# Kernel tuning notes

Measured on AMD Instinct MI355X. Metric: run time of the kernel, lower is better.

## Reference

```python
import jax, jax.numpy as jnp
import numpy as np

B, CIN, REL, OUT, SH, H, W = 8, 256, 16, 64, 8, 56, 56
HW = H * W
K = 7          # window size
DIL = 2        # dilation
EPS = 1e-5


def conv1x1(x, w, b=None):
    # x: [B,C,h,w], w: [O,C]
    y = jnp.einsum('oc,bchw->bohw', w, x)
    if b is not None:
        y = y + b[None, :, None, None]
    return y


def bn_eval(x, g, b, m, v):
    scale = g / jnp.sqrt(v + EPS)
    return x * scale[None, :, None, None] + (b - m * scale)[None, :, None, None]


def unfold49(x, pad_reflect, pad_zero):
    # x: [B,C,H,W] -> [B,C,49,H,W]; 7x7 window, dilation 2, stride 1.
    if pad_reflect:
        x = jnp.pad(x, ((0, 0), (0, 0), (pad_reflect, pad_reflect), (pad_reflect, pad_reflect)), mode='reflect')
    if pad_zero:
        x = jnp.pad(x, ((0, 0), (0, 0), (pad_zero, pad_zero), (pad_zero, pad_zero)))
    patches = [x[:, :, DIL * i:DIL * i + H, DIL * j:DIL * j + W]
               for i in range(K) for j in range(K)]
    return jnp.stack(patches, axis=2)


def setup_inputs() -> dict:
    key = jax.random.key(0)
    ks = jax.random.split(key, 12)
    s_in = 1.0 / np.sqrt(CIN)
    inp = {
        'x': jax.random.normal(ks[0], (B, CIN, H, W), jnp.float32),
        'w1': jax.random.normal(ks[1], (REL, CIN), jnp.float32) * s_in,
        'b1': jax.random.normal(ks[2], (REL,), jnp.float32) * 0.01,
        'w2': jax.random.normal(ks[3], (REL, CIN), jnp.float32) * s_in,
        'b2': jax.random.normal(ks[4], (REL,), jnp.float32) * 0.01,
        'w3': jax.random.normal(ks[5], (OUT, CIN), jnp.float32) * s_in,
        'b3': jax.random.normal(ks[6], (OUT,), jnp.float32) * 0.01,
        'bn1_g': jax.random.uniform(ks[7], (REL * (K * K + 1),), jnp.float32, 0.5, 1.5),
        'bn1_b': jax.random.normal(ks[8], (REL * (K * K + 1),), jnp.float32) * 0.01,
        'bn1_m': jnp.zeros((REL * (K * K + 1),), jnp.float32),
        'bn1_v': jnp.ones((REL * (K * K + 1),), jnp.float32),
        'wcw1': jax.random.normal(ks[9], (OUT // SH, REL * (K * K + 1)), jnp.float32) * (1.0 / np.sqrt(REL * 50)),
        'bn2_g': jax.random.uniform(ks[10], (OUT // SH,), jnp.float32, 0.5, 1.5),
        'bn2_b': jnp.zeros((OUT // SH,), jnp.float32),
        'bn2_m': jnp.zeros((OUT // SH,), jnp.float32),
        'bn2_v': jnp.ones((OUT // SH,), jnp.float32),
        'wcw2': jax.random.normal(ks[11], (K * K * OUT // SH, OUT // SH), jnp.float32) * (1.0 / np.sqrt(OUT // SH)),
        'bcw2': jnp.zeros((K * K * OUT // SH,), jnp.float32),
    }
    return inp


def reference(x, w1, b1, w2, b2, w3, b3, bn1_g, bn1_b, bn1_m, bn1_v,
              wcw1, bn2_g, bn2_b, bn2_m, bn2_v, wcw2, bcw2):
    x1 = conv1x1(x, w1, b1)                      # [B,REL,H,W]
    x2 = conv1x1(x, w2, b2)                      # [B,REL,H,W]
    x3 = conv1x1(x, w3, b3)                      # [B,OUT,H,W]

    # x1 -> [B,REL,1,HW]
    x1f = x1.reshape(B, REL, 1, HW)
    # x2: ReflectionPad2d(2) then Unfold(7, dilation=2, padding=4) -> [B,REL*49,1,HW]
    x2u = unfold49(x2, pad_reflect=2, pad_zero=4).reshape(B, REL * K * K, 1, HW)

    cat = jnp.concatenate([x1f, x2u], axis=1)    # [B, REL*50, 1, HW]
    t = jax.nn.relu(bn_eval(cat, bn1_g, bn1_b, bn1_m, bn1_v))
    t = conv1x1(t, wcw1)                         # [B, OUT/SH, 1, HW], no bias
    t = jax.nn.relu(bn_eval(t, bn2_g, bn2_b, bn2_m, bn2_v))
    wmap = conv1x1(t, wcw2, bcw2)                # [B, 49*OUT/SH, 1, HW]
    wmap = wmap.reshape(B, OUT // SH, K * K, HW)  # channel layout wc*49+k

    # Aggregation(7, 1, 6, 2, pad_mode=1): reflect-pad 6, 7x7 dilated unfold,
    # out[b,c,n] = sum_k unf[b,c,k,n] * w[b, c//SH, k, n]
    x3u = unfold49(x3, pad_reflect=6, pad_zero=0).reshape(B, OUT // SH, SH, K * K, HW)
    out = jnp.einsum('bgskn,bgkn->bgsn', x3u, wmap).reshape(B, OUT, H, W)
    return out
```

## Files before the change

kernel.cpp:

```cpp
#include <hip/hip_runtime.h>
#include <hip/hip_bf16.h>

#define HW    3136
#define HH    56
#define NCIN  256
#define KK    49
#define PH    68
#define PP    (PH*PH)

#define OFF_WT    0
#define OFF_BCAT  24576
#define OFF_SSH   24672
#define OFF_WC1T  26272
#define OFF_B2F   32672
#define OFF_X1    32768
#define OFF_X2P   434176
#define OFF_X3P   1026048
#define OFF_TB    3393536

__global__ __launch_bounds__(256) void kprep(
    const float* __restrict__ w1, const float* __restrict__ b1,
    const float* __restrict__ w2, const float* __restrict__ b2,
    const float* __restrict__ w3, const float* __restrict__ b3,
    const float* __restrict__ bn1g, const float* __restrict__ bn1b,
    const float* __restrict__ bn1m, const float* __restrict__ bn1v,
    const float* __restrict__ wcw1,
    const float* __restrict__ bn2g, const float* __restrict__ bn2b,
    const float* __restrict__ bn2m, const float* __restrict__ bn2v,
    float* __restrict__ ws)
{
    int idx = blockIdx.x * 256 + threadIdx.x;
    if (idx < 24576) {
        int o = idx >> 8, c = idx & 255;
        float v = (o < 16) ? w1[o * 256 + c]
                : (o < 32) ? w2[(o - 16) * 256 + c]
                           : w3[(o - 32) * 256 + c];
        ws[OFF_WT + c * 96 + o] = v;
    }
    int i2 = idx - 24576;
    if (i2 >= 0 && i2 < 96) {
        float v = (i2 < 16) ? b1[i2] : (i2 < 32) ? b2[i2 - 16] : b3[i2 - 32];
        ws[OFF_BCAT + i2] = v;
    }
    int i3 = idx - 24672;
    if (i3 >= 0 && i3 < 800) {
        float s = bn1g[i3] / sqrtf(bn1v[i3] + 1e-5f);
        ws[OFF_SSH + 2 * i3]     = s;
        ws[OFF_SSH + 2 * i3 + 1] = bn1b[i3] - bn1m[i3] * s;
    }
    int i4 = idx - 25472;
    if (i4 >= 0 && i4 < 6400) {
        int j = i4 >> 3, g = i4 & 7;
        float s2 = bn2g[g] / sqrtf(bn2v[g] + 1e-5f);
        ws[OFF_WC1T + i4] = wcw1[g * 800 + j] * s2;
    }
    int i5 = idx - 31872;
    if (i5 >= 0 && i5 < 8) {
        float s2 = bn2g[i5] / sqrtf(bn2v[i5] + 1e-5f);
        ws[OFF_B2F + i5] = bn2b[i5] - bn2m[i5] * s2;
    }
    int i6 = idx - 31880;
    if (i6 >= 0 && i6 < 8 * 16 * PP) {
        ws[OFF_X2P + i6] = 0.f;
    }
}

__global__ __launch_bounds__(512) void kconv(
    const float* __restrict__ x, const float* __restrict__ wT,
    const float* __restrict__ bcat, float* __restrict__ x1out,
    float* __restrict__ x2pad, float* __restrict__ x3pad)
{
    __shared__ float xl[64][64];
    const int tid = threadIdx.x;
    const int l   = tid & 63;
    const int wv  = __builtin_amdgcn_readfirstlane(tid >> 6);
    const int b   = blockIdx.x / 49;
    const int hw0 = (blockIdx.x % 49) * 64;
    const int ob  = wv * 12;

    float acc[12];
    const float* bc = bcat + ob;
#pragma unroll
    for (int i = 0; i < 12; ++i) acc[i] = bc[i];

    const float* xb = x + (size_t)b * NCIN * HW + hw0;

    for (int cc = 0; cc < 4; ++cc) {
        __syncthreads();
#pragma unroll
        for (int i = 0; i < 8; ++i)
            xl[i * 8 + wv][l] = xb[(size_t)(cc * 64 + i * 8 + wv) * HW + l];
        __syncthreads();

        const float* wp = wT + (cc * 64) * 96 + ob;
#pragma unroll 4
        for (int k = 0; k < 64; ++k) {
            float xv = xl[k][l];
            const float4* wq = (const float4*)(wp + k * 96);
            float4 A = wq[0], B = wq[1], C = wq[2];
            acc[0]  = fmaf(xv, A.x, acc[0]);  acc[1]  = fmaf(xv, A.y, acc[1]);
            acc[2]  = fmaf(xv, A.z, acc[2]);  acc[3]  = fmaf(xv, A.w, acc[3]);
            acc[4]  = fmaf(xv, B.x, acc[4]);  acc[5]  = fmaf(xv, B.y, acc[5]);
            acc[6]  = fmaf(xv, B.z, acc[6]);  acc[7]  = fmaf(xv, B.w, acc[7]);
            acc[8]  = fmaf(xv, C.x, acc[8]);  acc[9]  = fmaf(xv, C.y, acc[9]);
            acc[10] = fmaf(xv, C.z, acc[10]); acc[11] = fmaf(xv, C.w, acc[11]);
        }
    }

    const int n  = hw0 + l;
    const int y  = n / HH;
    const int xx = n - y * HH;
    const int p0 = y + 6, q0 = xx + 6;
    const int yr3 = (y >= 1 && y <= 6) ? 6 - y : ((y >= 49 && y <= 54) ? 116 - y : -1);
    const int xr3 = (xx >= 1 && xx <= 6) ? 6 - xx : ((xx >= 49 && xx <= 54) ? 116 - xx : -1);
    const int yr2 = (y == 1 || y == 2) ? 6 - y : ((y == 53 || y == 54) ? 116 - y : -1);
    const int xr2 = (xx == 1 || xx == 2) ? 6 - xx : ((xx == 53 || xx == 54) ? 116 - xx : -1);

#pragma unroll
    for (int i = 0; i < 12; ++i) {
        const int ch = ob + i;
        const float v = acc[i];
        if (ch < 16) {
            x1out[((size_t)b * 16 + ch) * HW + n] = v;
        } else if (ch < 32) {
            float* pl = x2pad + ((size_t)b * 16 + (ch - 16)) * PP;
            pl[p0 * PH + q0] = v;
            if (yr2 >= 0)              pl[yr2 * PH + q0]  = v;
            if (xr2 >= 0)              pl[p0 * PH + xr2]  = v;
            if (yr2 >= 0 && xr2 >= 0)  pl[yr2 * PH + xr2] = v;
        } else {
            float* pl = x3pad + ((size_t)b * 64 + (ch - 32)) * PP;
            pl[p0 * PH + q0] = v;
            if (yr3 >= 0)              pl[yr3 * PH + q0]  = v;
            if (xr3 >= 0)              pl[p0 * PH + xr3]  = v;
            if (yr3 >= 0 && xr3 >= 0)  pl[yr3 * PH + xr3] = v;
        }
    }
}

__global__ __launch_bounds__(512) void kt(
    const float* __restrict__ x1, const float* __restrict__ x2pad,
    const float* __restrict__ ssh, const float* __restrict__ wc1t,
    const float* __restrict__ b2f, float* __restrict__ tbuf)
{
    __shared__ float red[8][8][64];
    const int tid = threadIdx.x;
    const int w   = __builtin_amdgcn_readfirstlane(tid >> 6);
    const int l   = tid & 63;
    const int b   = blockIdx.x / 49;
    const int nb  = (blockIdx.x % 49) * 64;
    const int n   = nb + l;
    const int y   = n / HH;
    const int xx  = n - y * HH;
    const int pbase = y * PH + xx;

    const float* x1b = x1 + (size_t)b * 16 * HW + n;
    const float* x2b = x2pad + (size_t)b * 16 * PP + pbase;

    float acc[8];
#pragma unroll
    for (int g = 0; g < 8; ++g) acc[g] = 0.f;

    const int u0 = (50 * w) >> 3;
    const int u1 = (50 * (w + 1)) >> 3;

#pragma unroll 2
    for (int u = u0; u < u1; ++u) {
        if (u == 0) {
#pragma unroll
            for (int r = 0; r < 16; ++r) {
                float v = x1b[(size_t)r * HW];
                float2 ss = *(const float2*)(ssh + 2 * r);
                v = fmaxf(fmaf(v, ss.x, ss.y), 0.f);
                const float4* wq = (const float4*)(wc1t + r * 8);
                float4 A = wq[0], Bv = wq[1];
                acc[0] = fmaf(v, A.x, acc[0]);  acc[1] = fmaf(v, A.y, acc[1]);
                acc[2] = fmaf(v, A.z, acc[2]);  acc[3] = fmaf(v, A.w, acc[3]);
                acc[4] = fmaf(v, Bv.x, acc[4]); acc[5] = fmaf(v, Bv.y, acc[5]);
                acc[6] = fmaf(v, Bv.z, acc[6]); acc[7] = fmaf(v, Bv.w, acc[7]);
            }
        } else {
            const int kk = __builtin_amdgcn_readfirstlane(u - 1);
            const int i  = kk / 7;
            const int jj = kk - i * 7;
            const float* xp = x2b + i * (2 * PH) + jj * 2;
#pragma unroll
            for (int r = 0; r < 16; ++r) {
                const int j = 16 + r * KK + kk;
                float v = xp[(size_t)r * PP];
                float2 ss = *(const float2*)(ssh + 2 * j);
                v = fmaxf(fmaf(v, ss.x, ss.y), 0.f);
                const float4* wq = (const float4*)(wc1t + j * 8);
                float4 A = wq[0], Bv = wq[1];
                acc[0] = fmaf(v, A.x, acc[0]);  acc[1] = fmaf(v, A.y, acc[1]);
                acc[2] = fmaf(v, A.z, acc[2]);  acc[3] = fmaf(v, A.w, acc[3]);
                acc[4] = fmaf(v, Bv.x, acc[4]); acc[5] = fmaf(v, Bv.y, acc[5]);
                acc[6] = fmaf(v, Bv.z, acc[6]); acc[7] = fmaf(v, Bv.w, acc[7]);
            }
        }
    }

#pragma unroll
    for (int g = 0; g < 8; ++g) red[w][g][l] = acc[g];
    __syncthreads();

    {
        const int g  = tid >> 6;
        const int px = tid & 63;
        float s = b2f[g];
#pragma unroll
        for (int ww = 0; ww < 8; ++ww) s += red[ww][g][px];
        tbuf[((size_t)b * 8 + g) * HW + nb + px] = fmaxf(s, 0.f);
    }
}

__global__ __launch_bounds__(512) void kagg(
    const float* __restrict__ x3pad, const float* __restrict__ tbuf,
    const float* __restrict__ wcw2, const float* __restrict__ bcw2,
    float* __restrict__ out)
{
    const int tid  = threadIdx.x;
    const int g    = __builtin_amdgcn_readfirstlane(tid >> 6);
    const int lane = tid & 63;
    const int sh   = lane >> 5;
    const int pp   = lane & 31;
    const int b    = blockIdx.x / 49;
    const int nb   = (blockIdx.x % 49) * 64;
    const int n0   = nb + pp * 2;
    const int y    = n0 / HH;
    const int xx   = n0 - y * HH;
    const int pbase = y * PH + xx;

    float t0[8], t1[8];
#pragma unroll
    for (int e = 0; e < 8; ++e) {
        float2 tv = *(const float2*)(tbuf + ((size_t)b * 8 + e) * HW + n0);
        t0[e] = tv.x; t1[e] = tv.y;
    }

    float2 acc[4];
#pragma unroll
    for (int s = 0; s < 4; ++s) acc[s] = make_float2(0.f, 0.f);

    const float* x3b = x3pad + ((size_t)b * 64 + g * 8 + sh * 4) * PP + pbase;
    const float* wr  = wcw2 + (size_t)g * KK * 8;
    const float* br  = bcw2 + (size_t)g * KK;

#pragma unroll 1
    for (int i = 0; i < 7; ++i) {
        const float* xrow = x3b + i * (2 * PH);
#pragma unroll
        for (int jj = 0; jj < 7; ++jj) {
            const int k = i * 7 + jj;
            float w0 = br[k], w1 = w0;
            const float* wk = wr + k * 8;
#pragma unroll
            for (int e = 0; e < 8; ++e) {
                float we = wk[e];
                w0 = fmaf(t0[e], we, w0);
                w1 = fmaf(t1[e], we, w1);
            }
#pragma unroll
            for (int s = 0; s < 4; ++s) {
                float2 xv = *(const float2*)(xrow + (size_t)s * PP + jj * 2);
                acc[s].x = fmaf(xv.x, w0, acc[s].x);
                acc[s].y = fmaf(xv.y, w1, acc[s].y);
            }
        }
    }

    float* op = out + ((size_t)b * 64 + g * 8 + sh * 4) * HW + n0;
#pragma unroll
    for (int s = 0; s < 4; ++s)
        *(float2*)(op + (size_t)s * HW) = acc[s];
}

extern "C" void kernel_launch(void* const* d_in, const int* in_sizes, int n_in,
                              void* d_out, int out_size, void* d_ws, size_t ws_size,
                              hipStream_t stream) {
    const float* x    = (const float*)d_in[0];
    const float* w1   = (const float*)d_in[1];
    const float* b1   = (const float*)d_in[2];
    const float* w2   = (const float*)d_in[3];
    const float* b2   = (const float*)d_in[4];
    const float* w3   = (const float*)d_in[5];
    const float* b3   = (const float*)d_in[6];
    const float* bn1g = (const float*)d_in[7];
    const float* bn1b = (const float*)d_in[8];
    const float* bn1m = (const float*)d_in[9];
    const float* bn1v = (const float*)d_in[10];
    const float* wcw1 = (const float*)d_in[11];
    const float* bn2g = (const float*)d_in[12];
    const float* bn2b = (const float*)d_in[13];
    const float* bn2m = (const float*)d_in[14];
    const float* bn2v = (const float*)d_in[15];
    const float* wcw2 = (const float*)d_in[16];
    const float* bcw2 = (const float*)d_in[17];

    float* ws = (float*)d_ws;

    kprep<<<2437, 256, 0, stream>>>(w1, b1, w2, b2, w3, b3,
                                    bn1g, bn1b, bn1m, bn1v, wcw1,
                                    bn2g, bn2b, bn2m, bn2v, ws);
    kconv<<<392, 512, 0, stream>>>(x, ws + OFF_WT, ws + OFF_BCAT,
                                   ws + OFF_X1, ws + OFF_X2P, ws + OFF_X3P);
    kt<<<392, 512, 0, stream>>>(ws + OFF_X1, ws + OFF_X2P,
                                ws + OFF_SSH, ws + OFF_WC1T, ws + OFF_B2F,
                                ws + OFF_TB);
    kagg<<<392, 512, 0, stream>>>(ws + OFF_X3P, ws + OFF_TB, wcw2, bcw2,
                                  (float*)d_out);
}
```

Measured before the change: 77.78 us.

## Widen kt/kagg blocks to 1024 threads, pack weight tables, move pad zeroing into kconv

After: 81.42 us. 4.7% more time.

```diff
diff --git a/kernel.cpp b/kernel.cpp
--- a/kernel.cpp
+++ b/kernel.cpp
@@ -10,13 +10,13 @@
 
 #define OFF_WT    0
 #define OFF_BCAT  24576
-#define OFF_SSH   24672
-#define OFF_WC1T  26272
-#define OFF_B2F   32672
-#define OFF_X1    32768
-#define OFF_X2P   434176
-#define OFF_X3P   1026048
-#define OFF_TB    3393536
+#define OFF_TAB   24672
+#define OFF_WTAB  34272
+#define OFF_B2F   38976
+#define OFF_X1    39040
+#define OFF_X2P   440448
+#define OFF_X3P   1032320
+#define OFF_TB    3399808
 
 __global__ __launch_bounds__(256) void kprep(
     const float* __restrict__ w1, const float* __restrict__ b1,
@@ -27,6 +27,7 @@
     const float* __restrict__ wcw1,
     const float* __restrict__ bn2g, const float* __restrict__ bn2b,
     const float* __restrict__ bn2m, const float* __restrict__ bn2v,
+    const float* __restrict__ wcw2, const float* __restrict__ bcw2,
     float* __restrict__ ws)
 {
     int idx = blockIdx.x * 256 + threadIdx.x;
@@ -43,25 +44,35 @@
         ws[OFF_BCAT + i2] = v;
     }
     int i3 = idx - 24672;
-    if (i3 >= 0 && i3 < 800) {
-        float s = bn1g[i3] / sqrtf(bn1v[i3] + 1e-5f);
-        ws[OFF_SSH + 2 * i3]     = s;
-        ws[OFF_SSH + 2 * i3 + 1] = bn1b[i3] - bn1m[i3] * s;
-    }
-    int i4 = idx - 25472;
-    if (i4 >= 0 && i4 < 6400) {
-        int j = i4 >> 3, g = i4 & 7;
-        float s2 = bn2g[g] / sqrtf(bn2v[g] + 1e-5f);
-        ws[OFF_WC1T + i4] = wcw1[g * 800 + j] * s2;
-    }
-    int i5 = idx - 31872;
+    if (i3 >= 0 && i3 < 9600) {
+        int row = i3 / 12, c = i3 - row * 12;
+        int uu = row >> 4, r = row & 15;
+        int j = (uu < 49) ? (16 + r * KK + uu) : r;
+        float val = 0.f;
+        if (c == 0) {
+            val = bn1g[j] / sqrtf(bn1v[j] + 1e-5f);
+        } else if (c == 1) {
+            float s = bn1g[j] / sqrtf(bn1v[j] + 1e-5f);
+            val = bn1b[j] - bn1m[j] * s;
+        } else if (c < 10) {
+            int e = c - 2;
+            float s2 = bn2g[e] / sqrtf(bn2v[e] + 1e-5f);
+            val = wcw1[e * 800 + j] * s2;
+        }
+        ws[OFF_TAB + i3] = val;
+    }
+    int i4 = idx - 34272;
+    if (i4 >= 0 && i4 < 4704) {
+        int row = i4 / 12, c = i4 - row * 12;
+        float val = 0.f;
+        if (c == 0)      val = bcw2[row];
+        else if (c < 9)  val = wcw2[row * 8 + (c - 1)];
+        ws[OFF_WTAB + i4] = val;
+    }
+    int i5 = idx - 38976;
     if (i5 >= 0 && i5 < 8) {
         float s2 = bn2g[i5] / sqrtf(bn2v[i5] + 1e-5f);
         ws[OFF_B2F + i5] = bn2b[i5] - bn2m[i5] * s2;
-    }
-    int i6 = idx - 31880;
-    if (i6 >= 0 && i6 < 8 * 16 * PP) {
-        ws[OFF_X2P + i6] = 0.f;
     }
 }
 
@@ -77,6 +88,18 @@
     const int b   = blockIdx.x / 49;
     const int hw0 = (blockIdx.x % 49) * 64;
     const int ob  = wv * 12;
+
+    {
+        int z = (blockIdx.x % 49) * 336 + tid;
+        if (tid < 336 && z < 16384) {
+            int ch = z >> 10, cell = z & 1023;
+            int p, q;
+            if (cell < 272)      { p = cell / 68;          q = cell - p * 68; }
+            else if (cell < 544) { int cc = cell - 272; p = 64 + cc / 68; q = cc - (p - 64) * 68; }
+            else                 { int cc = cell - 544; p = 4 + (cc >> 3); int qq = cc & 7; q = (qq < 4) ? qq : 60 + qq; }
+            x2pad[((size_t)b * 16 + ch) * PP + p * PH + q] = 0.f;
+        }
+    }
 
     float acc[12];
     const float* bc = bcat + ob;
@@ -138,12 +161,12 @@
     }
 }
 
-__global__ __launch_bounds__(512) void kt(
+__global__ __launch_bounds__(1024, 8) void kt(
     const float* __restrict__ x1, const float* __restrict__ x2pad,
-    const float* __restrict__ ssh, const float* __restrict__ wc1t,
-    const float* __restrict__ b2f, float* __restrict__ tbuf)
+    const float* __restrict__ tab, const float* __restrict__ b2f,
+    float* __restrict__ tbuf)
 {
-    __shared__ float red[8][8][64];
+    __shared__ float red[16][8][64];
     const int tid = threadIdx.x;
     const int w   = __builtin_amdgcn_readfirstlane(tid >> 6);
     const int l   = tid & 63;
@@ -161,42 +184,36 @@
 #pragma unroll
     for (int g = 0; g < 8; ++g) acc[g] = 0.f;
 
-    const int u0 = (50 * w) >> 3;
-    const int u1 = (50 * (w + 1)) >> 3;
-
-#pragma unroll 2
+    const int u0 = (50 * w) >> 4;
+    const int u1 = (50 * (w + 1)) >> 4;
+
+#pragma unroll 1
     for (int u = u0; u < u1; ++u) {
+        const float* trow;
+        const float* xp;
+        size_t xstr;
         if (u == 0) {
-#pragma unroll
-            for (int r = 0; r < 16; ++r) {
-                float v = x1b[(size_t)r * HW];
-                float2 ss = *(const float2*)(ssh + 2 * r);
-                v = fmaxf(fmaf(v, ss.x, ss.y), 0.f);
-                const float4* wq = (const float4*)(wc1t + r * 8);
-                float4 A = wq[0], Bv = wq[1];
-                acc[0] = fmaf(v, A.x, acc[0]);  acc[1] = fmaf(v, A.y, acc[1]);
-                acc[2] = fmaf(v, A.z, acc[2]);  acc[3] = fmaf(v, A.w, acc[3]);
-                acc[4] = fmaf(v, Bv.x, acc[4]); acc[5] = fmaf(v, Bv.y, acc[5]);
-                acc[6] = fmaf(v, Bv.z, acc[6]); acc[7] = fmaf(v, Bv.w, acc[7]);
-            }
+            trow = tab + 49 * 192;
+            xp   = x1b;
+            xstr = HW;
         } else {
-            const int kk = __builtin_amdgcn_readfirstlane(u - 1);
+            const int kk = u - 1;
             const int i  = kk / 7;
             const int jj = kk - i * 7;
-            const float* xp = x2b + i * (2 * PH) + jj * 2;
-#pragma unroll
-            for (int r = 0; r < 16; ++r) {
-                const int j = 16 + r * KK + kk;
-                float v = xp[(size_t)r * PP];
-                float2 ss = *(const float2*)(ssh + 2 * j);
-                v = fmaxf(fmaf(v, ss.x, ss.y), 0.f);
-                const float4* wq = (const float4*)(wc1t + j * 8);
-                float4 A = wq[0], Bv = wq[1];
-                acc[0] = fmaf(v, A.x, acc[0]);  acc[1] = fmaf(v, A.y, acc[1]);
-                acc[2] = fmaf(v, A.z, acc[2]);  acc[3] = fmaf(v, A.w, acc[3]);
-                acc[4] = fmaf(v, Bv.x, acc[4]); acc[5] = fmaf(v, Bv.y, acc[5]);
-                acc[6] = fmaf(v, Bv.z, acc[6]); acc[7] = fmaf(v, Bv.w, acc[7]);
-            }
+            trow = tab + kk * 192;
+            xp   = x2b + i * (2 * PH) + jj * 2;
+            xstr = PP;
+        }
+#pragma unroll
+        for (int r = 0; r < 16; ++r) {
+            const float4* tq = (const float4*)(trow + r * 12);
+            float4 A = tq[0], Bv = tq[1], Cv = tq[2];
+            float v = xp[(size_t)r * xstr];
+            v = fmaxf(fmaf(v, A.x, A.y), 0.f);
+            acc[0] = fmaf(v, A.z, acc[0]);  acc[1] = fmaf(v, A.w, acc[1]);
+            acc[2] = fmaf(v, Bv.x, acc[2]); acc[3] = fmaf(v, Bv.y, acc[3]);
+            acc[4] = fmaf(v, Bv.z, acc[4]); acc[5] = fmaf(v, Bv.w, acc[5]);
+            acc[6] = fmaf(v, Cv.x, acc[6]); acc[7] = fmaf(v, Cv.y, acc[7]);
         }
     }
 
@@ -204,75 +221,78 @@
     for (int g = 0; g < 8; ++g) red[w][g][l] = acc[g];
     __syncthreads();
 
-    {
+    if (tid < 512) {
         const int g  = tid >> 6;
         const int px = tid & 63;
         float s = b2f[g];
 #pragma unroll
-        for (int ww = 0; ww < 8; ++ww) s += red[ww][g][px];
+        for (int sl = 0; sl < 16; ++sl) s += red[sl][g][px];
         tbuf[((size_t)b * 8 + g) * HW + nb + px] = fmaxf(s, 0.f);
     }
 }
 
-__global__ __launch_bounds__(512) void kagg(
+__global__ __launch_bounds__(1024, 8) void kagg(
     const float* __restrict__ x3pad, const float* __restrict__ tbuf,
-    const float* __restrict__ wcw2, const float* __restrict__ bcw2,
-    float* __restrict__ out)
+    const float* __restrict__ wtab, float* __restrict__ out)
 {
+    __shared__ float red[8][8][64];
     const int tid  = threadIdx.x;
-    const int g    = __builtin_amdgcn_readfirstlane(tid >> 6);
-    const int lane = tid & 63;
-    const int sh   = lane >> 5;
-    const int pp   = lane & 31;
+    const int wave = tid >> 6;
+    const int g    = __builtin_amdgcn_readfirstlane(wave & 7);
+    const int kh   = __builtin_amdgcn_readfirstlane(wave >> 3);
+    const int l    = tid & 63;
     const int b    = blockIdx.x / 49;
     const int nb   = (blockIdx.x % 49) * 64;
-    const int n0   = nb + pp * 2;
-    const int y    = n0 / HH;
-    const int xx   = n0 - y * HH;
+    const int n    = nb + l;
+    const int y    = n / HH;
+    const int xx   = n - y * HH;
     const int pbase = y * PH + xx;
 
-    float t0[8], t1[8];
-#pragma unroll
-    for (int e = 0; e < 8; ++e) {
-        float2 tv = *(const float2*)(tbuf + ((size_t)b * 8 + e) * HW + n0);
-        t0[e] = tv.x; t1[e] = tv.y;
-    }
-
-    float2 acc[4];
-#pragma unroll
-    for (int s = 0; s < 4; ++s) acc[s] = make_float2(0.f, 0.f);
-
-    const float* x3b = x3pad + ((size_t)b * 64 + g * 8 + sh * 4) * PP + pbase;
-    const float* wr  = wcw2 + (size_t)g * KK * 8;
-    const float* br  = bcw2 + (size_t)g * KK;
+    float t[8];
+#pragma unroll
+    for (int e = 0; e < 8; ++e) t[e] = tbuf[((size_t)b * 8 + e) * HW + n];
+
+    float acc[8];
+#pragma unroll
+    for (int s = 0; s < 8; ++s) acc[s] = 0.f;
+
+    const float* x3b = x3pad + ((size_t)b * 64 + g * 8) * PP + pbase;
+    const float* wg  = wtab + (size_t)g * KK * 12;
+
+    const int k0 = kh * 25;
+    const int k1 = kh ? KK : 25;
 
 #pragma unroll 1
-    for (int i = 0; i < 7; ++i) {
-        const float* xrow = x3b + i * (2 * PH);
-#pragma unroll
-        for (int jj = 0; jj < 7; ++jj) {
-            const int k = i * 7 + jj;
-            float w0 = br[k], w1 = w0;
-            const float* wk = wr + k * 8;
-#pragma unroll
-            for (int e = 0; e < 8; ++e) {
-                float we = wk[e];
-                w0 = fmaf(t0[e], we, w0);
-                w1 = fmaf(t1[e], we, w1);
-            }
-#pragma unroll
-            for (int s = 0; s < 4; ++s) {
-                float2 xv = *(const float2*)(xrow + (size_t)s * PP + jj * 2);
-                acc[s].x = fmaf(xv.x, w0, acc[s].x);
-                acc[s].y = fmaf(xv.y, w1, acc[s].y);
-            }
-        }
-    }
-
-    float* op = out + ((size_t)b * 64 + g * 8 + sh * 4) * HW + n0;
-#pragma unroll
-    for (int s = 0; s < 4; ++s)
-        *(float2*)(op + (size_t)s * HW) = acc[s];
+    for (int k = k0; k < k1; ++k) {
+        const int i  = k / 7;
+        const int jj = k - i * 7;
+        const float* wrow = wg + k * 12;
+        const float4* wq = (const float4*)wrow;
+        float4 A = wq[0], Bv = wq[1];
+        float w7 = wrow[8];
+        float wv = A.x;
+        wv = fmaf(t[0], A.y, wv);  wv = fmaf(t[1], A.z, wv);
+        wv = fmaf(t[2], A.w, wv);  wv = fmaf(t[3], Bv.x, wv);
+        wv = fmaf(t[4], Bv.y, wv); wv = fmaf(t[5], Bv.z, wv);
+        wv = fmaf(t[6], Bv.w, wv); wv = fmaf(t[7], w7, wv);
+
+        const float* xp = x3b + i * (2 * PH) + jj * 2;
+#pragma unroll
+        for (int s = 0; s < 8; ++s)
+            acc[s] = fmaf(xp[(size_t)s * PP], wv, acc[s]);
+    }
+
+    if (kh == 1) {
+#pragma unroll
+        for (int s = 0; s < 8; ++s) red[g][s][l] = acc[s];
+    }
+    __syncthreads();
+    if (kh == 0) {
+        float* op = out + ((size_t)b * 64 + g * 8) * HW + n;
+#pragma unroll
+        for (int s = 0; s < 8; ++s)
+            op[(size_t)s * HW] = acc[s] + red[g][s][l];
+    }
 }
 
 extern "C" void kernel_launch(void* const* d_in, const int* in_sizes, int n_in,
@@ -299,14 +319,13 @@
 
     float* ws = (float*)d_ws;
 
-    kprep<<<2437, 256, 0, stream>>>(w1, b1, w2, b2, w3, b3,
-                                    bn1g, bn1b, bn1m, bn1v, wcw1,
-                                    bn2g, bn2b, bn2m, bn2v, ws);
+    kprep<<<153, 256, 0, stream>>>(w1, b1, w2, b2, w3, b3,
+                                   bn1g, bn1b, bn1m, bn1v, wcw1,
+                                   bn2g, bn2b, bn2m, bn2v, wcw2, bcw2, ws);
     kconv<<<392, 512, 0, stream>>>(x, ws + OFF_WT, ws + OFF_BCAT,
                                    ws + OFF_X1, ws + OFF_X2P, ws + OFF_X3P);
-    kt<<<392, 512, 0, stream>>>(ws + OFF_X1, ws + OFF_X2P,
-                                ws + OFF_SSH, ws + OFF_WC1T, ws + OFF_B2F,
-                                ws + OFF_TB);
-    kagg<<<392, 512, 0, stream>>>(ws + OFF_X3P, ws + OFF_TB, wcw2, bcw2,
-                                  (float*)d_out);
-}
+    kt<<<392, 1024, 0, stream>>>(ws + OFF_X1, ws + OFF_X2P,
+                                 ws + OFF_TAB, ws + OFF_B2F, ws + OFF_TB);
+    kagg<<<392, 1024, 0, stream>>>(ws + OFF_X3P, ws + OFF_TB,
+                                   ws + OFF_WTAB, (float*)d_out);
+}
```
